# Optimization experiments

Hardware: AMD Instinct MI355X
Metric: run time of the kernel (lower is better)

The kernel has to match this reference:

```python
import jax, jax.numpy as jnp
import numpy as np

H, W, C = 2160, 3840, 3
K = 1  # kernel_size (splat radius window)


def setup_inputs() -> dict:
    key = jax.random.key(0)
    k1, k2, k3 = jax.random.split(key, 3)
    img = jax.random.normal(k1, (H, W, C), dtype=jnp.float32)
    flow = jax.random.normal(k2, (1, H, W, 2), dtype=jnp.float32) * 4.0  # dx, dy
    depth = jax.random.uniform(k3, (H, W), dtype=jnp.float32, minval=0.1, maxval=10.0)
    return {"img": img, "flow": flow, "depth": depth}


def reference(img, flow, depth):
    """Forward flow-based splatting with per-pixel depth z-buffer test.

    Each source pixel (y,x) is splatted to round((x,y) + flow) within a
    K x K kernel window; where multiple sources land on the same target
    pixel, the one with the smallest depth wins (z-buffer).
    """
    h, w, c = img.shape
    f = flow[0]  # [h, w, 2]
    xs = jnp.arange(w, dtype=f.dtype)
    ys = jnp.arange(h, dtype=f.dtype)
    tx0 = xs[None, :] + f[..., 0]  # target x, [h, w]
    ty0 = ys[:, None] + f[..., 1]  # target y, [h, w]

    offs = [(dy, dx)
            for dy in range(-(K // 2), (K - 1) // 2 + 1)
            for dx in range(-(K // 2), (K - 1) // 2 + 1)]

    dflat = depth.reshape(-1)            # [h*w]
    img_flat = img.reshape(-1, c)        # [h*w, c]

    idx_list, dep_list, src_list = [], [], []
    for dy, dx in offs:
        tx = jnp.round(tx0 + dx).astype(jnp.int32)
        ty = jnp.round(ty0 + dy).astype(jnp.int32)
        valid = (tx >= 0) & (tx < w) & (ty >= 0) & (ty < h)
        lin = jnp.where(valid, ty * w + tx, -1).reshape(-1)  # -1 -> dropped
        idx_list.append(lin)
        dep_list.append(dflat)
        src_list.append(img_flat)

    idx = jnp.concatenate(idx_list)   # [n_splats]
    dep = jnp.concatenate(dep_list)   # [n_splats]
    src = jnp.concatenate(src_list)   # [n_splats, c]

    # Pass 1: scatter-min depth into z-buffer (out-of-bounds dropped).
    zbuf = jnp.full(h * w, jnp.inf, dtype=dep.dtype).at[idx].min(dep, mode='drop')
    # Pass 2: only the depth-test winners write their color.
    win = (dep <= zbuf[jnp.clip(idx, 0, h * w - 1)]) & (idx >= 0)
    widx = jnp.where(win, idx, -1)
    out = jnp.zeros((h * w, c), dtype=img.dtype).at[widx].add(
        src * win[:, None].astype(src.dtype), mode='drop')
    return out.reshape(h, w, c)
```

## Files before the change

### kernel.cpp

```cpp
#include <hip/hip_runtime.h>

constexpr int H = 2160, W = 3840;
constexpr int NPIX = H * W;
constexpr int M = 20;
constexpr int TW = 64, TH = 32;
constexpr int TS = TW * TH;
constexpr int WW = TW + 2 * M;
constexpr int TXN = W / TW;
constexpr int TYN = (H + TH - 1) / TH;
constexpr int NTILES = TXN * TYN;
constexpr int BLK = 512;
constexpr int QROW = WW / 4;
constexpr int RPP = BLK / QROW;
constexpr unsigned long long EMPTY = ~0ULL;
constexpr unsigned FAR_CAP = 65536;
static_assert(WW % 4 == 0 && RPP * 4 >= TH + 2 * M, "sweep geometry");

typedef float f32x4 __attribute__((ext_vector_type(4)));



__global__ void __launch_bounds__(256)
prep_kernel(const f32x4* __restrict__ flow4, const float4* __restrict__ depth4,
            uint4* __restrict__ tgt16_4,
            unsigned long long* __restrict__ overlay,
            unsigned int* __restrict__ farcount,
            unsigned int* __restrict__ dirty,
            uint4* __restrict__ farlist)
{
    int tid8 = blockIdx.x * 256 + threadIdx.x;
    unsigned long long oobkey = EMPTY;
    if (tid8 < NPIX / 8) {
        int i0 = tid8 * 8;
        int y  = i0 / W;
        int x0 = i0 - y * W;
        int q0 = tid8 * 2;
        f32x4 fa0 = __builtin_nontemporal_load(&flow4[q0 * 2]);
        f32x4 fa1 = __builtin_nontemporal_load(&flow4[q0 * 2 + 1]);
        f32x4 fb0 = __builtin_nontemporal_load(&flow4[q0 * 2 + 2]);
        f32x4 fb1 = __builtin_nontemporal_load(&flow4[q0 * 2 + 3]);
        float4 d0 = depth4[q0];
        float4 d1 = depth4[q0 + 1];
        float fx[8] = {fa0.x, fa0.z, fa1.x, fa1.z, fb0.x, fb0.z, fb1.x, fb1.z};
        float fy[8] = {fa0.y, fa0.w, fa1.y, fa1.w, fb0.y, fb0.w, fb1.y, fb1.w};
        float dz[8] = {d0.x, d0.y, d0.z, d0.w, d1.x, d1.y, d1.z, d1.w};
        unsigned short tv[8];
        #pragma unroll
        for (int c = 0; c < 8; ++c) {
            int x = x0 + c;
            int tx = (int)rintf((float)x + fx[c]);
            int ty = (int)rintf((float)y + fy[c]);
            bool valid = ((unsigned)tx < (unsigned)W) && ((unsigned)ty < (unsigned)H);
            unsigned short t = 0xFFFFu;
            if (!valid) {
                unsigned db = __float_as_uint(dz[c]);
                unsigned long long k =
                    ((unsigned long long)db << 32) | 0x80000000u | (unsigned)(i0 + c);
                oobkey = k < oobkey ? k : oobkey;
                dirty[NTILES - 1] = 1;
            } else {
                int dx = tx - x, dy = ty - y;
                bool far = ((unsigned)(dx + M) > (unsigned)(2 * M)) ||
                           ((unsigned)(dy + M) > (unsigned)(2 * M));
                if (far) {
                    unsigned db  = __float_as_uint(dz[c]);
                    int lin = ty * W + tx;
                    unsigned long long key =
                        ((unsigned long long)db << 32) | (unsigned)(i0 + c);
                    atomicMin(&overlay[lin], key);
                    dirty[(ty / TH) * TXN + (tx / TW)] = 1;
                    unsigned slot = atomicAdd(farcount, 1u);
                    if (slot < FAR_CAP)
                        farlist[slot] = make_uint4((unsigned)lin, db,
                                                   (unsigned)(i0 + c), 0u);
                } else {
                    t = (unsigned short)(((dy + M) << 6) | (dx + M));
                }
            }
            tv[c] = t;
        }
        uint4 sv;
        sv.x = (unsigned)tv[0] | ((unsigned)tv[1] << 16);
        sv.y = (unsigned)tv[2] | ((unsigned)tv[3] << 16);
        sv.z = (unsigned)tv[4] | ((unsigned)tv[5] << 16);
        sv.w = (unsigned)tv[6] | ((unsigned)tv[7] << 16);
        tgt16_4[tid8] = sv;
    }
    #pragma unroll
    for (int o = 32; o > 0; o >>= 1) {
        unsigned long long other = __shfl_down(oobkey, o);
        oobkey = other < oobkey ? other : oobkey;
    }
    if ((threadIdx.x & 63) == 0 && oobkey != EMPTY)
        atomicMin(&overlay[NPIX - 1], oobkey);
}

__global__ void __launch_bounds__(BLK, 8)
resolve_kernel(const unsigned short* __restrict__ tgt16,
               const float* __restrict__ depth,
               const float* __restrict__ img,
               const unsigned long long* __restrict__ overlay,
               const unsigned int* __restrict__ dirty,
               const unsigned int* __restrict__ farcount,
               const uint4* __restrict__ farlist,
               float* __restrict__ out)
{
    __shared__ unsigned long long lkey[TS];
    __shared__ int lflag;
    const int tid = threadIdx.x;
    const int tile = (blockIdx.x % 8) * (NTILES / 8) + blockIdx.x / 8;
    const int tyi = tile / TXN, txi = tile - tyi * TXN;
    const int ty0 = tyi * TH, tx0 = txi * TW;
    const bool isdirty = dirty[tile] != 0;

    const int wy_lo = max(ty0 - M, 0);
    const int wy_hi = min(ty0 + TH + M, H);
    const int nrows = wy_hi - wy_lo;
    const int nwin  = nrows * WW;
    const int myrow = tid / QROW;
    const int myq   = tid - myrow * QROW;
    const int gxb   = tx0 - M + myq * 4;
    const bool qok  = (myrow < RPP) && ((unsigned)gxb < (unsigned)W);

    auto LOADR = [&](int pass, ushort4& t4, float4& d4) -> bool {
        int row = pass * RPP + myrow;
        bool act = qok && (row < nrows);
        int gy  = wy_lo + min(row, nrows - 1);
        int gxc = min(max(gxb, 0), W - 4);
        size_t base = (size_t)gy * W + gxc;
        t4 = *(const ushort4*)(&tgt16[base]);
        d4 = *(const float4*)(&depth[base]);
        return act;
    };
    auto PROCR = [&](int pass, bool act, ushort4 t4, float4 d4) {
        if (!act) return;
        int gy = wy_lo + pass * RPP + myrow;
        unsigned tt[4] = {t4.x, t4.y, t4.z, t4.w};
        float    dz[4] = {d4.x, d4.y, d4.z, d4.w};
        #pragma unroll
        for (int c = 0; c < 4; ++c) {
            unsigned t = tt[c];
            int gx = gxb + c;
            int tx = gx + (int)(t & 63u) - M;
            int ty = gy + (int)(t >> 6) - M;
            unsigned ltx = (unsigned)(tx - tx0);
            unsigned lty = (unsigned)(ty - ty0);
            if (ltx >= (unsigned)TW || lty >= (unsigned)TH) continue;
            unsigned p  = lty * TW + ltx;
            unsigned gi = (unsigned)(gy * W + gx);
            unsigned long long key =
                ((unsigned long long)__float_as_uint(dz[c]) << 32) | gi;
            unsigned long long old = atomicMin(&lkey[p], key);
            if ((unsigned)(old >> 32) == (unsigned)(key >> 32) && old != key)
                lflag = 1;
        }
    };

    ushort4 ta, tb; float4 da, db_;
    bool actA = LOADR(0, ta, da);
    bool actB = LOADR(1, tb, db_);

    #pragma unroll
    for (int pp = 0; pp < TS / BLK; ++pp) lkey[pp * BLK + tid] = EMPTY;
    if (tid == 0) lflag = 0;
    __syncthreads();

    PROCR(0, actA, ta, da);
    bool actC = LOADR(2, ta, da);
    PROCR(1, actB, tb, db_);
    bool actD = LOADR(3, tb, db_);
    PROCR(2, actC, ta, da);
    PROCR(3, actD, tb, db_);
    __syncthreads();

    #pragma unroll
    for (int pp = 0; pp < TS / BLK; ++pp) {
        int p = pp * BLK + tid;
        int ly = p >> 6, lx = p & 63;
        int gy = ty0 + ly, gx = tx0 + lx;
        if (gy >= H) continue;
        int gi = gy * W + gx;
        unsigned long long k = lkey[p];
        if (isdirty) {
            unsigned long long o = overlay[gi];
            if ((o >> 32) == (k >> 32) && o != k && k != EMPTY) lflag = 1;
            if (o < k) { k = o; lkey[p] = k; }
        }
        float r = 0.f, g = 0.f, b = 0.f;
        if (k != EMPTY && !((unsigned)k & 0x80000000u)) {
            int src = (int)((unsigned)k & 0x7FFFFFFFu);
            r = img[3 * src + 0];
            g = img[3 * src + 1];
            b = img[3 * src + 2];
        }
        __builtin_nontemporal_store(r, &out[3 * gi + 0]);
        __builtin_nontemporal_store(g, &out[3 * gi + 1]);
        __builtin_nontemporal_store(b, &out[3 * gi + 2]);
    }
    __syncthreads();

    if (isdirty) {
        unsigned n = *farcount;
        if (n > FAR_CAP) n = FAR_CAP;
        for (unsigned r = tid; r < n; r += BLK) {
            uint4 rec = farlist[r];
            unsigned ty = rec.x / (unsigned)W;
            unsigned tx = rec.x - ty * (unsigned)W;
            if ((int)(ty / TH) != tyi || (int)(tx / TW) != txi) continue;
            unsigned p = (ty - (unsigned)ty0) * TW + (tx - (unsigned)tx0);
            unsigned long long k = lkey[p];
            if ((unsigned)(k >> 32) == rec.y && ((unsigned)k & 0x7FFFFFFFu) != rec.z) {
                atomicAdd(&out[3 * rec.x + 0], img[3 * rec.z + 0]);
                atomicAdd(&out[3 * rec.x + 1], img[3 * rec.z + 1]);
                atomicAdd(&out[3 * rec.x + 2], img[3 * rec.z + 2]);
            }
        }
    }

    if (lflag) {
        const int wx_lo = tx0 - M;
        for (int j = tid; j < nwin; j += BLK) {
            int wy = j / WW;
            int wx = j - wy * WW;
            int gy = wy_lo + wy;
            int gx = wx_lo + wx;
            if ((unsigned)gx >= (unsigned)W) continue;
            int gi = gy * W + gx;
            unsigned t = tgt16[gi];
            int tx = gx + (int)(t & 63u) - M;
            int ty = gy + (int)(t >> 6) - M;
            unsigned ltx = (unsigned)(tx - tx0);
            unsigned lty = (unsigned)(ty - ty0);
            if (ltx >= (unsigned)TW || lty >= (unsigned)TH) continue;
            unsigned long long k = lkey[lty * TW + ltx];
            unsigned db = __float_as_uint(depth[gi]);
            if ((unsigned)(k >> 32) == db && ((unsigned)k & 0x7FFFFFFFu) != (unsigned)gi) {
                int lin = ty * W + tx;
                atomicAdd(&out[3 * lin + 0], img[3 * gi + 0]);
                atomicAdd(&out[3 * lin + 1], img[3 * gi + 1]);
                atomicAdd(&out[3 * lin + 2], img[3 * gi + 2]);
            }
        }
    }
}


__global__ void __launch_bounds__(256)
fb_zmin(const float2* __restrict__ flow, const float* __restrict__ depth,
        unsigned long long* __restrict__ zbuf)
{
    int i = blockIdx.x * 256 + threadIdx.x;
    if (i >= NPIX) return;
    int y = i / W, x = i - y * W;
    float2 f = flow[i];
    int tx = (int)rintf((float)x + f.x);
    int ty = (int)rintf((float)y + f.y);
    bool valid = (tx >= 0) && (tx < W) && (ty >= 0) && (ty < H);
    int lin = valid ? (ty * W + tx) : (NPIX - 1);
    unsigned db = __float_as_uint(depth[i]);
    unsigned long long key = ((unsigned long long)db << 32) | (unsigned)i | (valid ? 0u : 0x80000000u);
    if (zbuf[lin] > key) atomicMin(&zbuf[lin], key);
}

__global__ void __launch_bounds__(256)
fb_gather(const unsigned long long* __restrict__ zbuf,
          const float* __restrict__ img, float* __restrict__ out)
{
    int t = blockIdx.x * 256 + threadIdx.x;
    if (t >= NPIX) return;
    unsigned long long key = zbuf[t];
    float r = 0.f, g = 0.f, b = 0.f;
    if (key != EMPTY && !((unsigned)key & 0x80000000u)) {
        int src = (int)((unsigned)key & 0x7FFFFFFFu);
        r = img[3 * src + 0]; g = img[3 * src + 1]; b = img[3 * src + 2];
    }
    out[3 * t + 0] = r; out[3 * t + 1] = g; out[3 * t + 2] = b;
}

__global__ void __launch_bounds__(256)
fb_tiefix(const float2* __restrict__ flow, const float* __restrict__ depth,
          const float* __restrict__ img,
          const unsigned long long* __restrict__ zbuf, float* __restrict__ out)
{
    int i = blockIdx.x * 256 + threadIdx.x;
    if (i >= NPIX) return;
    int y = i / W, x = i - y * W;
    float2 f = flow[i];
    int tx = (int)rintf((float)x + f.x);
    int ty = (int)rintf((float)y + f.y);
    if (tx < 0 || tx >= W || ty < 0 || ty >= H) return;
    int lin = ty * W + tx;
    unsigned long long key = zbuf[lin];
    unsigned db = __float_as_uint(depth[i]);
    if (db == (unsigned)(key >> 32) && (unsigned)key != (unsigned)i) {
        atomicAdd(&out[3 * lin + 0], img[3 * i + 0]);
        atomicAdd(&out[3 * lin + 1], img[3 * i + 1]);
        atomicAdd(&out[3 * lin + 2], img[3 * i + 2]);
    }
}

extern "C" void kernel_launch(void* const* d_in, const int* in_sizes, int n_in,
                              void* d_out, int out_size, void* d_ws, size_t ws_size,
                              hipStream_t stream) {
    const float*  img   = (const float*)d_in[0];
    const float2* flow  = (const float2*)d_in[1];
    const float*  depth = (const float*)d_in[2];
    float* out = (float*)d_out;
    char* ws = (char*)d_ws;

    const size_t off_overlay = (size_t)NPIX * 2;
    const size_t off_meta    = off_overlay + (size_t)NPIX * 8;
    const size_t off_dirty   = off_meta + 16;
    const size_t off_far     = off_dirty + (size_t)NTILES * 4;
    const size_t need = off_far + (size_t)FAR_CAP * 16;

    dim3 blk(256), grd((NPIX + 255) / 256);

    if (ws_size >= need) {
        uint4*              tgt16_4  = (uint4*)ws;
        unsigned long long* overlay  = (unsigned long long*)(ws + off_overlay);
        unsigned int*       farcount = (unsigned int*)(ws + off_meta);
        unsigned int*       dirtyf   = (unsigned int*)(ws + off_dirty);
        uint4*              farlist  = (uint4*)(ws + off_far);

        hipMemsetAsync(ws + off_meta, 0, 16 + (size_t)NTILES * 4, stream);

        prep_kernel<<<dim3(NPIX / 8 / 256), blk, 0, stream>>>(
            (const f32x4*)flow, (const float4*)depth, tgt16_4, overlay,
            farcount, dirtyf, farlist);
        resolve_kernel<<<dim3(NTILES), dim3(BLK), 0, stream>>>(
            (const unsigned short*)ws, depth, img, overlay, dirtyf,
            farcount, farlist, out);
    } else {
        unsigned long long* zbuf = (unsigned long long*)ws;
        hipMemsetAsync(zbuf, 0xFF, (size_t)NPIX * 8, stream);
        fb_zmin  <<<grd, blk, 0, stream>>>(flow, depth, zbuf);
        fb_gather<<<grd, blk, 0, stream>>>(zbuf, img, out);
        fb_tiefix<<<grd, blk, 0, stream>>>(flow, depth, img, zbuf, out);
    }
}
```

Before: 91.89 us.

## Widen splat tiles to 128 columns with 8-pixel per-thread loads

Tile width doubles from 64 to 128 columns, which shrinks the relative halo overhead of the 20-pixel margin around each tile. Each thread now loads and processes 8 consecutive source pixels instead of 4, so the window sweep needs three row passes instead of four. Clamping at the image edges makes some threads re-process overlapping pixels; this is harmless for the atomicMin keys but costs a little extra LDS atomic traffic. Fewer, larger blocks, with LDS per block doubled to 32 KB, may lower occupancy and parallelism.

```diff
diff --git a/kernel.cpp b/kernel.cpp
--- a/kernel.cpp
+++ b/kernel.cpp
@@ -3,18 +3,18 @@
 constexpr int H = 2160, W = 3840;
 constexpr int NPIX = H * W;
 constexpr int M = 20;
-constexpr int TW = 64, TH = 32;
+constexpr int TW = 128, TH = 32;
 constexpr int TS = TW * TH;
 constexpr int WW = TW + 2 * M;
 constexpr int TXN = W / TW;
 constexpr int TYN = (H + TH - 1) / TH;
 constexpr int NTILES = TXN * TYN;
 constexpr int BLK = 512;
-constexpr int QROW = WW / 4;
-constexpr int RPP = BLK / QROW;
+constexpr int OROW = WW / 8;
+constexpr int RPP = BLK / OROW;
 constexpr unsigned long long EMPTY = ~0ULL;
 constexpr unsigned FAR_CAP = 65536;
-static_assert(WW % 4 == 0 && RPP * 4 >= TH + 2 * M, "sweep geometry");
+static_assert(WW % 8 == 0 && RPP * 3 >= TH + 2 * M, "sweep geometry");
 
 typedef float f32x4 __attribute__((ext_vector_type(4)));
 
@@ -117,30 +117,34 @@
     const int wy_hi = min(ty0 + TH + M, H);
     const int nrows = wy_hi - wy_lo;
     const int nwin  = nrows * WW;
-    const int myrow = tid / QROW;
-    const int myq   = tid - myrow * QROW;
-    const int gxb   = tx0 - M + myq * 4;
-    const bool qok  = (myrow < RPP) && ((unsigned)gxb < (unsigned)W);
-
-    auto LOADR = [&](int pass, ushort4& t4, float4& d4) -> bool {
+    const int myrow = tid / OROW;
+    const int myo   = tid - myrow * OROW;
+    const int gxb   = tx0 - M + myo * 8;
+    const int gxc   = min(max(gxb, 0), W - 8);
+    const bool ook  = (myrow < RPP) && (gxb > -8) && (gxb < W);
+
+    auto LOADR = [&](int pass, ushort4& t4a, ushort4& t4b,
+                     float4& d4a, float4& d4b) -> bool {
         int row = pass * RPP + myrow;
-        bool act = qok && (row < nrows);
-        int gy  = wy_lo + min(row, nrows - 1);
-        int gxc = min(max(gxb, 0), W - 4);
+        bool act = ook && (row < nrows);
+        int gy = wy_lo + min(row, nrows - 1);
         size_t base = (size_t)gy * W + gxc;
-        t4 = *(const ushort4*)(&tgt16[base]);
-        d4 = *(const float4*)(&depth[base]);
+        t4a = *(const ushort4*)(&tgt16[base]);
+        t4b = *(const ushort4*)(&tgt16[base + 4]);
+        d4a = *(const float4*)(&depth[base]);
+        d4b = *(const float4*)(&depth[base + 4]);
         return act;
     };
-    auto PROCR = [&](int pass, bool act, ushort4 t4, float4 d4) {
+    auto PROCR = [&](int pass, bool act, ushort4 t4a, ushort4 t4b,
+                     float4 d4a, float4 d4b) {
         if (!act) return;
         int gy = wy_lo + pass * RPP + myrow;
-        unsigned tt[4] = {t4.x, t4.y, t4.z, t4.w};
-        float    dz[4] = {d4.x, d4.y, d4.z, d4.w};
+        unsigned tt[8] = {t4a.x, t4a.y, t4a.z, t4a.w, t4b.x, t4b.y, t4b.z, t4b.w};
+        float    dz[8] = {d4a.x, d4a.y, d4a.z, d4a.w, d4b.x, d4b.y, d4b.z, d4b.w};
         #pragma unroll
-        for (int c = 0; c < 4; ++c) {
+        for (int c = 0; c < 8; ++c) {
             unsigned t = tt[c];
-            int gx = gxb + c;
+            int gx = gxc + c;
             int tx = gx + (int)(t & 63u) - M;
             int ty = gy + (int)(t >> 6) - M;
             unsigned ltx = (unsigned)(tx - tx0);
@@ -156,27 +160,25 @@
         }
     };
 
-    ushort4 ta, tb; float4 da, db_;
-    bool actA = LOADR(0, ta, da);
-    bool actB = LOADR(1, tb, db_);
+    ushort4 ta0, ta1, tb0, tb1; float4 da0, da1, db0, db1;
+    bool actA = LOADR(0, ta0, ta1, da0, da1);
+    bool actB = LOADR(1, tb0, tb1, db0, db1);
 
     #pragma unroll
     for (int pp = 0; pp < TS / BLK; ++pp) lkey[pp * BLK + tid] = EMPTY;
     if (tid == 0) lflag = 0;
     __syncthreads();
 
-    PROCR(0, actA, ta, da);
-    bool actC = LOADR(2, ta, da);
-    PROCR(1, actB, tb, db_);
-    bool actD = LOADR(3, tb, db_);
-    PROCR(2, actC, ta, da);
-    PROCR(3, actD, tb, db_);
+    PROCR(0, actA, ta0, ta1, da0, da1);
+    bool actC = LOADR(2, ta0, ta1, da0, da1);
+    PROCR(1, actB, tb0, tb1, db0, db1);
+    PROCR(2, actC, ta0, ta1, da0, da1);
     __syncthreads();
 
     #pragma unroll
     for (int pp = 0; pp < TS / BLK; ++pp) {
         int p = pp * BLK + tid;
-        int ly = p >> 6, lx = p & 63;
+        int ly = p >> 7, lx = p & 127;
         int gy = ty0 + ly, gx = tx0 + lx;
         if (gy >= H) continue;
         int gi = gy * W + gx;
```

New measurement: 94.35 us. +2.7%, slower.
